# Kernel tuning notes

Hardware: AMD Instinct MI355X
Metric: run time of the kernel (lower is better)

Reference implementation:

```python
import jax, jax.numpy as jnp
import numpy as np

T, N, HIDDEN = 2048, 4, 512
N_HEAD = 8
D_HEAD = HIDDEN // N_HEAD
# Faithful to torch buffer: 1.0 / hidden_size ** d_head -> underflows to 0.0
SCALE = np.float32(1.0 / (HIDDEN ** D_HEAD))
LN_EPS = 1e-5


def _layernorm(x, g, b):
    m = jnp.mean(x, axis=-1, keepdims=True)
    v = jnp.mean(jnp.square(x - m), axis=-1, keepdims=True)
    return (x - m) * jax.lax.rsqrt(v + LN_EPS) * g + b


def setup_inputs() -> dict:
    key = jax.random.key(0)
    ks = jax.random.split(key, 6)
    s = 0.02
    return {
        "x": jax.random.normal(ks[0], (T, N, HIDDEN), jnp.float32),
        "qkv_w": jax.random.normal(ks[1], (HIDDEN, 3 * HIDDEN), jnp.float32) * s,
        "qkv_b": jnp.zeros((3 * HIDDEN,), jnp.float32),
        "out_w": jax.random.normal(ks[2], (HIDDEN, HIDDEN), jnp.float32) * s,
        "out_b": jnp.zeros((HIDDEN,), jnp.float32),
        "ln1_g": jnp.ones((HIDDEN,), jnp.float32),
        "ln1_b": jnp.zeros((HIDDEN,), jnp.float32),
        "ff1_w": jax.random.normal(ks[3], (HIDDEN, 2 * HIDDEN), jnp.float32) * s,
        "ff1_b": jnp.zeros((2 * HIDDEN,), jnp.float32),
        "ff2_w": jax.random.normal(ks[4], (2 * HIDDEN, HIDDEN), jnp.float32) * s,
        "ff2_b": jnp.zeros((HIDDEN,), jnp.float32),
        "ln2_g": jnp.ones((HIDDEN,), jnp.float32),
        "ln2_b": jnp.zeros((HIDDEN,), jnp.float32),
    }


def reference(x, qkv_w, qkv_b, out_w, out_b, ln1_g, ln1_b,
              ff1_w, ff1_b, ff2_w, ff2_b, ln2_g, ln2_b):
    t, n, _ = x.shape
    # prenorm=True path, dropout_p=0 (identity)
    residual = x
    h = _layernorm(x, ln1_g, ln1_b)
    qkv = h @ qkv_w + qkv_b  # [t, n, 3*hidden]
    q, k, v = jnp.split(qkv, 3, axis=2)
    q = q.reshape(t, n, N_HEAD, D_HEAD)
    k = k.reshape(t, n, N_HEAD, D_HEAD)
    v = v.reshape(t, n, N_HEAD, D_HEAD)
    logits = jnp.einsum('ibhd,jbhd->ijbh', q, k)
    probs = jax.nn.softmax(logits * SCALE, axis=1)
    attn_out = jnp.einsum('ijbh,jbhd->ibhd', probs, v).reshape(t, n, HIDDEN)
    x = residual + (attn_out @ out_w + out_b)
    residual = x
    h = _layernorm(x, ln2_g, ln2_b)
    ff = jnp.maximum(h @ ff1_w + ff1_b, 0.0) @ ff2_w + ff2_b
    return residual + ff
```

## Files before the change

### kernel.cpp

```cpp
#include <hip/hip_runtime.h>
#include <math.h>


#define DEVI __device__ __forceinline__

typedef unsigned short u16;
typedef unsigned int   u32;
using short8 = __attribute__((ext_vector_type(8))) short;
using f32x4  = __attribute__((ext_vector_type(4))) float;

constexpr int T_ = 2048;
constexpr int NB = 4;
constexpr int H  = 512;
constexpr int M  = T_ * NB;
constexpr int FF = 2 * H;
constexpr float LN_EPS = 1e-5f;

DEVI u16 f2bf(float f) {
    union { float f; u32 u; } v; v.f = f;
    u32 r = v.u + 0x7FFFu + ((v.u >> 16) & 1u);
    return (u16)(r >> 16);
}

DEVI void gload16(const u16* src, u16* lds) {
    __builtin_amdgcn_global_load_lds(
        (const __attribute__((address_space(1))) u32*)src,
        (__attribute__((address_space(3))) u32*)lds, 16, 0, 0);
}

DEVI float hsum8(const float4& a, const float4& b) {
    return a.x + a.y + a.z + a.w + b.x + b.y + b.z + b.w;
}
DEVI float hsq8(const float4& a, const float4& b) {
    return a.x*a.x + a.y*a.y + a.z*a.z + a.w*a.w +
           b.x*b.x + b.y*b.y + b.z*b.z + b.w*b.w;
}
DEVI float4 ln_apply(const float4& v, float mean, float rs,
                     const float4& g, const float4& b) {
    float4 r;
    r.x = (v.x - mean) * rs * g.x + b.x;
    r.y = (v.y - mean) * rs * g.y + b.y;
    r.z = (v.z - mean) * rs * g.z + b.z;
    r.w = (v.w - mean) * rs * g.w + b.w;
    return r;
}
DEVI void add4(float4& a, const float4& b) {
    a.x += b.x; a.y += b.y; a.z += b.z; a.w += b.w;
}
DEVI void wave_reduce2(float& s, float& q) {
    #pragma unroll
    for (int m = 1; m < 64; m <<= 1) {
        s += __shfl_xor(s, m, 64);
        q += __shfl_xor(q, m, 64);
    }
}

__global__ __launch_bounds__(256) void k_prep(
    const float* __restrict__ W1, const float* __restrict__ W2,
    u16* __restrict__ w1f, u16* __restrict__ w2f, float* __restrict__ mh)
{
    __shared__ float tile[32][33];
    const int t = threadIdx.x;
    const int bid = blockIdx.x;

    if (bid == 0) {
        for (int i = t; i < NB * H; i += 256) mh[i] = 0.f;
    }

    const float* W;
    u16* Wf;
    int K, N, k0, n0;
    if (bid < 512) {
        W = W1; Wf = w1f; K = H; N = FF;
        k0 = (bid & 15) * 32;  n0 = (bid >> 4) * 32;
    } else {
        const int b2 = bid - 512;
        W = W2; Wf = w2f; K = FF; N = H;
        k0 = (b2 & 31) * 32;   n0 = (b2 >> 5) * 32;
    }

    #pragma unroll
    for (int i = 0; i < 4; ++i) {
        const int idx = t + i * 256;
        const int r = idx >> 5, c = idx & 31;
        tile[r][c] = W[(size_t)(k0 + r) * N + n0 + c];
    }
    __syncthreads();
    if (t < 128) {
        const int tt = t >> 6;
        const int c  = t & 63;
        short8 o;
        #pragma unroll
        for (int kin = 0; kin < 8; ++kin)
            o[kin] = f2bf(tile[(c >> 4) * 8 + kin][tt * 16 + (c & 15)]);
        const size_t idx = (((size_t)(n0 / 16 + tt) * (K >> 5) + (k0 >> 5)) << 9)
                         + c * 8;
        *(short8*)&Wf[idx] = o;
    }
}

__global__ __launch_bounds__(256) void k_ln1_atomic(
    const float* __restrict__ x, const float* __restrict__ g,
    const float* __restrict__ be, float* __restrict__ mh)
{
    const int lane = threadIdx.x & 63;
    const int w    = threadIdx.x >> 6;
    const int t0   = blockIdx.x * 8;

    const float4* G4 = (const float4*)g;
    const float4* B4 = (const float4*)be;
    const float4 g0 = G4[lane], g1 = G4[64 + lane];
    const float4 b0 = B4[lane], b1 = B4[64 + lane];

    float4 acc0 = {0, 0, 0, 0}, acc1 = {0, 0, 0, 0};
    for (int i = 0; i < 8; ++i) {
        const int r = (t0 + i) * NB + w;
        const float4* X4 = (const float4*)(x + (size_t)r * H);
        float4 v0 = X4[lane], v1 = X4[64 + lane];
        float s = hsum8(v0, v1);
        float q = hsq8(v0, v1);
        wave_reduce2(s, q);
        const float mean = s * (1.0f / H);
        const float var  = q * (1.0f / H) - mean * mean;
        const float rs   = 1.0f / sqrtf(var + LN_EPS);
        add4(acc0, ln_apply(v0, mean, rs, g0, b0));
        add4(acc1, ln_apply(v1, mean, rs, g1, b1));
    }
    float* dst = mh + (size_t)w * H;
    atomicAdd(&dst[lane * 4 + 0],       acc0.x);
    atomicAdd(&dst[lane * 4 + 1],       acc0.y);
    atomicAdd(&dst[lane * 4 + 2],       acc0.z);
    atomicAdd(&dst[lane * 4 + 3],       acc0.w);
    atomicAdd(&dst[256 + lane * 4 + 0], acc1.x);
    atomicAdd(&dst[256 + lane * 4 + 1], acc1.y);
    atomicAdd(&dst[256 + lane * 4 + 2], acc1.z);
    atomicAdd(&dst[256 + lane * 4 + 3], acc1.w);
}

__global__ __launch_bounds__(256) void k_gemv_coal(
    const float* __restrict__ vec, const float* __restrict__ W,
    const float* __restrict__ bias, float* __restrict__ outv,
    const int Kd, const int stride, const int colofs, const float vscale)
{
    __shared__ float red[16][17];
    const int t  = threadIdx.x;
    const int b  = blockIdx.x >> 5;
    const int j0 = (blockIdx.x & 31) * 16;
    const int jj = t & 15, ks = t >> 4;

    const float* vp = vec + (size_t)b * Kd + ks * 32;
    const float* wp = W + (size_t)(ks * 32) * stride + colofs + j0 + jj;
    float acc = 0.f;
    #pragma unroll 8
    for (int i = 0; i < 32; ++i)
        acc = fmaf(vp[i] * vscale, wp[(size_t)i * stride], acc);

    red[ks][jj] = acc;
    __syncthreads();
    if (t < 16) {
        float s = 0.f;
        #pragma unroll
        for (int k2 = 0; k2 < 16; ++k2) s += red[k2][t];
        outv[(size_t)b * 512 + j0 + t] = s + bias[j0 + t];
    }
}

__global__ __launch_bounds__(256) void k_ln2(
    const float* __restrict__ x, const float* __restrict__ cvec,
    const float* __restrict__ g, const float* __restrict__ be,
    u16* __restrict__ h2f)
{
    const int lane = threadIdx.x & 63;
    const int w    = threadIdx.x >> 6;
    const int r    = blockIdx.x * 4 + w;
    const int b    = r & 3;

    const float4* X4 = (const float4*)(x + (size_t)r * H);
    const float4* C4 = (const float4*)(cvec + (size_t)b * H);
    float4 v0 = X4[lane * 2],     v1 = X4[lane * 2 + 1];
    add4(v0, C4[lane * 2]);
    add4(v1, C4[lane * 2 + 1]);

    float s = hsum8(v0, v1);
    float q = hsq8(v0, v1);
    wave_reduce2(s, q);
    const float mean = s * (1.0f / H);
    const float var  = q * (1.0f / H) - mean * mean;
    const float rs   = 1.0f / sqrtf(var + LN_EPS);

    const float4* G4 = (const float4*)g;
    const float4* B4 = (const float4*)be;
    float4 h0 = ln_apply(v0, mean, rs, G4[lane * 2],     B4[lane * 2]);
    float4 h1 = ln_apply(v1, mean, rs, G4[lane * 2 + 1], B4[lane * 2 + 1]);

    short8 o;
    o[0] = f2bf(h0.x); o[1] = f2bf(h0.y); o[2] = f2bf(h0.z); o[3] = f2bf(h0.w);
    o[4] = f2bf(h1.x); o[5] = f2bf(h1.y); o[6] = f2bf(h1.z); o[7] = f2bf(h1.w);

    const size_t idx = (((size_t)(r >> 4) * 16 + (lane >> 2)) << 9)
                     + ((lane & 3) * 16 + (r & 15)) * 8;
    *(short8*)&h2f[idx] = o;
}

template<int MODE>
__global__ __launch_bounds__(256) void gemm_bf16(
    const u16* __restrict__ Af, const u16* __restrict__ Bf,
    const float* __restrict__ bias,
    const float* __restrict__ resid_x, const float* __restrict__ resid_c,
    float* __restrict__ outf, u16* __restrict__ outfrag,
    const int K, const int N)
{
    constexpr int BM = 128, BN = 128, BK = 64;
    const int KT = K >> 5;
    __shared__ alignas(16) u16 As[BM * BK];
    __shared__ alignas(16) u16 Bs[BN * BK];

    const int t    = threadIdx.x;
    const int lane = t & 63, w = t >> 6;
    const int wr = w >> 1, wc = w & 1;
    const int lr = lane & 15, lk = lane >> 4;
    const int bmt = blockIdx.x * 8;
    const int bnt = blockIdx.y * 8;

    f32x4 acc[4][4];
    #pragma unroll
    for (int i = 0; i < 4; ++i)
        #pragma unroll
        for (int j = 0; j < 4; ++j)
            acc[i][j] = (f32x4){0.f, 0.f, 0.f, 0.f};

    for (int kt0 = 0; kt0 < KT; kt0 += 2) {
        __syncthreads();
        #pragma unroll
        for (int ft = 0; ft < 4; ++ft) {
            const int f = ft * 256 + t;
            const int mt = f >> 7, ktl = (f >> 6) & 1, c = f & 63;
            gload16(Af + (((size_t)(bmt + mt) * KT + kt0 + ktl) << 9) + c * 8,
                    &As[f * 8]);
        }
        #pragma unroll
        for (int ft = 0; ft < 4; ++ft) {
            const int f = ft * 256 + t;
            const int nt = f >> 7, ktl = (f >> 6) & 1, c = f & 63;
            gload16(Bf + (((size_t)(bnt + nt) * KT + kt0 + ktl) << 9) + c * 8,
                    &Bs[f * 8]);
        }
        __syncthreads();

        #pragma unroll
        for (int ktl = 0; ktl < 2; ++ktl) {
            short8 a[4], b[4];
            #pragma unroll
            for (int i = 0; i < 4; ++i)
                a[i] = *(const short8*)&As[(((wr * 4 + i) * 2 + ktl) << 9) + lane * 8];
            #pragma unroll
            for (int j = 0; j < 4; ++j)
                b[j] = *(const short8*)&Bs[(((wc * 4 + j) * 2 + ktl) << 9) + lane * 8];
            #pragma unroll
            for (int i = 0; i < 4; ++i)
                #pragma unroll
                for (int j = 0; j < 4; ++j)
                    acc[i][j] = __builtin_amdgcn_mfma_f32_16x16x32_bf16(
                        a[i], b[j], acc[i][j], 0, 0, 0);
        }
    }

    const int K2T = N >> 5;
    #pragma unroll
    for (int i = 0; i < 4; ++i) {
        const int rt   = bmt + wr * 4 + i;
        const int row0 = rt * 16 + lk * 4;
        #pragma unroll
        for (int j = 0; j < 4; ++j) {
            const int col = (bnt + wc * 4 + j) * 16 + lr;
            const float bv = bias[col];
            #pragma unroll
            for (int r = 0; r < 4; ++r) {
                const int row = row0 + r;
                float v = acc[i][j][r] + bv;
                if (MODE == 0) {
                    v = fmaxf(v, 0.f);
                    const size_t idx =
                        (((size_t)rt * K2T + (col >> 5)) << 9)
                        + (((col >> 3) & 3) * 16 + (lk * 4 + r)) * 8
                        + (col & 7);
                    outfrag[idx] = f2bf(v);
                } else {
                    v += resid_x[(size_t)row * N + col]
                       + resid_c[(row & 3) * N + col];
                    outf[(size_t)row * N + col] = v;
                }
            }
        }
    }
}

extern "C" void kernel_launch(void* const* d_in, const int* in_sizes, int n_in,
                              void* d_out, int out_size, void* d_ws, size_t ws_size,
                              hipStream_t stream)
{
    const float* x     = (const float*)d_in[0];
    const float* qkv_w = (const float*)d_in[1];
    const float* qkv_b = (const float*)d_in[2];
    const float* out_w = (const float*)d_in[3];
    const float* out_b = (const float*)d_in[4];
    const float* ln1_g = (const float*)d_in[5];
    const float* ln1_b = (const float*)d_in[6];
    const float* ff1_w = (const float*)d_in[7];
    const float* ff1_b = (const float*)d_in[8];
    const float* ff2_w = (const float*)d_in[9];
    const float* ff2_b = (const float*)d_in[10];
    const float* ln2_g = (const float*)d_in[11];
    const float* ln2_b = (const float*)d_in[12];

    float* out = (float*)d_out;

    float* fws   = (float*)d_ws;
    float* mh    = fws;
    float* vmean = mh + NB * H;
    float* cvec  = vmean + NB * H;
    u16*   h2f   = (u16*)(cvec + NB * H);
    u16*   f1f   = h2f + (size_t)M * H;
    u16*   w1f   = f1f + (size_t)M * FF;
    u16*   w2f   = w1f + (size_t)H * FF;

    k_prep<<<1024, 256, 0, stream>>>(ff1_w, ff2_w, w1f, w2f, mh);

    k_ln1_atomic<<<256, 256, 0, stream>>>(x, ln1_g, ln1_b, mh);

    k_gemv_coal<<<128, 256, 0, stream>>>(mh, qkv_w, qkv_b + 2 * H, vmean,
                                         H, 3 * H, 2 * H, 1.0f / T_);
    k_gemv_coal<<<128, 256, 0, stream>>>(vmean, out_w, out_b, cvec,
                                         H, H, 0, 1.0f);

    k_ln2<<<M / 4, 256, 0, stream>>>(x, cvec, ln2_g, ln2_b, h2f);

    gemm_bf16<0><<<dim3(M / 128, FF / 128), 256, 0, stream>>>(
        h2f, w1f, ff1_b, nullptr, nullptr, nullptr, f1f, H, FF);

    gemm_bf16<1><<<dim3(M / 128, H / 128), 256, 0, stream>>>(
        f1f, w2f, ff2_b, x, cvec, out, nullptr, FF, H);
}
```

Measured before the change: 176.9 us.

## Merge prep kernels into one launch and precompute fused V·out weight

Combines the weight conversion, LN1 column-sum reduction, and a new precomputation of Wv@Wout (plus the fused bias) into a single multi-role kernel. Atomics are replaced by per-chunk partial sums that a new gemv kernel reduces. That kernel then applies the fused 512x512 weight in one pass instead of two chained gemvs. This cuts four launches down to two and removes the serial gemv dependency. The cost is an extra 512^3 FLOP fp32 matmul on every call and a 256-chunk partial reduction per batch column.

```diff
diff --git a/kernel.cpp b/kernel.cpp
--- a/kernel.cpp
+++ b/kernel.cpp
@@ -15,6 +15,7 @@
 constexpr int M  = T_ * NB;
 constexpr int FF = 2 * H;
 constexpr float LN_EPS = 1e-5f;
+constexpr int NCHUNK = 256;
 
 DEVI u16 f2bf(float f) {
     union { float f; u32 u; } v; v.f = f;
@@ -55,105 +56,156 @@
     }
 }
 
-__global__ __launch_bounds__(256) void k_prep(
+constexpr int NW1  = 512;
+constexpr int NW2  = 512;
+constexpr int NWE  = 256;
+constexpr int NBE  = 2;
+constexpr int NLN  = 256;
+constexpr int MEGA_BLOCKS = NW1 + NW2 + NWE + NBE + NLN;
+
+__global__ __launch_bounds__(256) void k_mega(
     const float* __restrict__ W1, const float* __restrict__ W2,
-    u16* __restrict__ w1f, u16* __restrict__ w2f, float* __restrict__ mh)
-{
-    __shared__ float tile[32][33];
-    const int t = threadIdx.x;
+    const float* __restrict__ qkv_w, const float* __restrict__ qkv_b,
+    const float* __restrict__ out_w, const float* __restrict__ out_b,
+    const float* __restrict__ x, const float* __restrict__ ln1g,
+    const float* __restrict__ ln1b,
+    u16* __restrict__ w1f, u16* __restrict__ w2f,
+    float* __restrict__ Weff, float* __restrict__ beff,
+    float* __restrict__ partials)
+{
+    __shared__ float smem[2 * 32 * 33];
+    const int t   = threadIdx.x;
     const int bid = blockIdx.x;
 
-    if (bid == 0) {
-        for (int i = t; i < NB * H; i += 256) mh[i] = 0.f;
-    }
-
-    const float* W;
-    u16* Wf;
-    int K, N, k0, n0;
-    if (bid < 512) {
-        W = W1; Wf = w1f; K = H; N = FF;
-        k0 = (bid & 15) * 32;  n0 = (bid >> 4) * 32;
+    if (bid < NW1 + NW2) {
+        const float* W;
+        u16* Wf;
+        int K, N, k0, n0;
+        if (bid < NW1) {
+            W = W1; Wf = w1f; K = H; N = FF;
+            k0 = (bid & 15) * 32;  n0 = (bid >> 4) * 32;
+        } else {
+            const int b2 = bid - NW1;
+            W = W2; Wf = w2f; K = FF; N = H;
+            k0 = (b2 & 31) * 32;   n0 = (b2 >> 5) * 32;
+        }
+        #pragma unroll
+        for (int i = 0; i < 4; ++i) {
+            const int idx = t + i * 256;
+            const int r = idx >> 5, c = idx & 31;
+            smem[r * 33 + c] = W[(size_t)(k0 + r) * N + n0 + c];
+        }
+        __syncthreads();
+        if (t < 128) {
+            const int tt = t >> 6;
+            const int c  = t & 63;
+            short8 o;
+            #pragma unroll
+            for (int kin = 0; kin < 8; ++kin)
+                o[kin] = f2bf(smem[((c >> 4) * 8 + kin) * 33 + tt * 16 + (c & 15)]);
+            const size_t idx =
+                (((size_t)(n0 / 16 + tt) * (K >> 5) + (k0 >> 5)) << 9) + c * 8;
+            *(short8*)&Wf[idx] = o;
+        }
+    } else if (bid < NW1 + NW2 + NWE) {
+        const int b3 = bid - (NW1 + NW2);
+        const int kt = b3 & 15, jt = b3 >> 4;
+        float* Av = smem;
+        float* Bo = smem + 32 * 33;
+        const int r  = t >> 3;
+        const int c4 = (t & 7) * 4;
+        float acc[4] = {0.f, 0.f, 0.f, 0.f};
+        for (int qt = 0; qt < 16; ++qt) {
+            #pragma unroll
+            for (int i = 0; i < 4; ++i) {
+                const int idx = t + i * 256;
+                const int rr = idx >> 5, cc = idx & 31;
+                Av[rr * 33 + cc] =
+                    qkv_w[(size_t)(kt * 32 + rr) * 1536 + 1024 + qt * 32 + cc];
+                Bo[rr * 33 + cc] =
+                    out_w[(size_t)(qt * 32 + rr) * 512 + jt * 32 + cc];
+            }
+            __syncthreads();
+            #pragma unroll 8
+            for (int q = 0; q < 32; ++q) {
+                const float a = Av[r * 33 + q];
+                acc[0] = fmaf(a, Bo[q * 33 + c4 + 0], acc[0]);
+                acc[1] = fmaf(a, Bo[q * 33 + c4 + 1], acc[1]);
+                acc[2] = fmaf(a, Bo[q * 33 + c4 + 2], acc[2]);
+                acc[3] = fmaf(a, Bo[q * 33 + c4 + 3], acc[3]);
+            }
+            __syncthreads();
+        }
+        #pragma unroll
+        for (int i = 0; i < 4; ++i)
+            Weff[(size_t)(kt * 32 + r) * 512 + jt * 32 + c4 + i] = acc[i];
+    } else if (bid < NW1 + NW2 + NWE + NBE) {
+        const int j = (bid - (NW1 + NW2 + NWE)) * 256 + t;
+        smem[t]       = qkv_b[1024 + t];
+        smem[256 + t] = qkv_b[1280 + t];
+        __syncthreads();
+        float acc = out_b[j];
+        #pragma unroll 8
+        for (int k = 0; k < 512; ++k)
+            acc = fmaf(smem[k], out_w[(size_t)k * 512 + j], acc);
+        beff[j] = acc;
     } else {
-        const int b2 = bid - 512;
-        W = W2; Wf = w2f; K = FF; N = H;
-        k0 = (b2 & 31) * 32;   n0 = (b2 >> 5) * 32;
-    }
-
-    #pragma unroll
-    for (int i = 0; i < 4; ++i) {
-        const int idx = t + i * 256;
-        const int r = idx >> 5, c = idx & 31;
-        tile[r][c] = W[(size_t)(k0 + r) * N + n0 + c];
-    }
-    __syncthreads();
-    if (t < 128) {
-        const int tt = t >> 6;
-        const int c  = t & 63;
-        short8 o;
-        #pragma unroll
-        for (int kin = 0; kin < 8; ++kin)
-            o[kin] = f2bf(tile[(c >> 4) * 8 + kin][tt * 16 + (c & 15)]);
-        const size_t idx = (((size_t)(n0 / 16 + tt) * (K >> 5) + (k0 >> 5)) << 9)
-                         + c * 8;
-        *(short8*)&Wf[idx] = o;
-    }
-}
-
-__global__ __launch_bounds__(256) void k_ln1_atomic(
-    const float* __restrict__ x, const float* __restrict__ g,
-    const float* __restrict__ be, float* __restrict__ mh)
-{
-    const int lane = threadIdx.x & 63;
-    const int w    = threadIdx.x >> 6;
-    const int t0   = blockIdx.x * 8;
-
-    const float4* G4 = (const float4*)g;
-    const float4* B4 = (const float4*)be;
-    const float4 g0 = G4[lane], g1 = G4[64 + lane];
-    const float4 b0 = B4[lane], b1 = B4[64 + lane];
-
-    float4 acc0 = {0, 0, 0, 0}, acc1 = {0, 0, 0, 0};
-    for (int i = 0; i < 8; ++i) {
-        const int r = (t0 + i) * NB + w;
-        const float4* X4 = (const float4*)(x + (size_t)r * H);
-        float4 v0 = X4[lane], v1 = X4[64 + lane];
-        float s = hsum8(v0, v1);
-        float q = hsq8(v0, v1);
-        wave_reduce2(s, q);
-        const float mean = s * (1.0f / H);
-        const float var  = q * (1.0f / H) - mean * mean;
-        const float rs   = 1.0f / sqrtf(var + LN_EPS);
-        add4(acc0, ln_apply(v0, mean, rs, g0, b0));
-        add4(acc1, ln_apply(v1, mean, rs, g1, b1));
-    }
-    float* dst = mh + (size_t)w * H;
-    atomicAdd(&dst[lane * 4 + 0],       acc0.x);
-    atomicAdd(&dst[lane * 4 + 1],       acc0.y);
-    atomicAdd(&dst[lane * 4 + 2],       acc0.z);
-    atomicAdd(&dst[lane * 4 + 3],       acc0.w);
-    atomicAdd(&dst[256 + lane * 4 + 0], acc1.x);
-    atomicAdd(&dst[256 + lane * 4 + 1], acc1.y);
-    atomicAdd(&dst[256 + lane * 4 + 2], acc1.z);
-    atomicAdd(&dst[256 + lane * 4 + 3], acc1.w);
-}
-
-__global__ __launch_bounds__(256) void k_gemv_coal(
-    const float* __restrict__ vec, const float* __restrict__ W,
-    const float* __restrict__ bias, float* __restrict__ outv,
-    const int Kd, const int stride, const int colofs, const float vscale)
-{
+        const int lb   = bid - (NW1 + NW2 + NWE + NBE);
+        const int lane = t & 63;
+        const int w    = t >> 6;
+        const int t0   = lb * 8;
+
+        const float4* G4 = (const float4*)ln1g;
+        const float4* B4 = (const float4*)ln1b;
+        const float4 g0 = G4[lane], g1 = G4[64 + lane];
+        const float4 b0 = B4[lane], b1 = B4[64 + lane];
+
+        float4 acc0 = {0, 0, 0, 0}, acc1 = {0, 0, 0, 0};
+        for (int i = 0; i < 8; ++i) {
+            const int r = (t0 + i) * NB + w;
+            const float4* X4 = (const float4*)(x + (size_t)r * H);
+            float4 v0 = X4[lane], v1 = X4[64 + lane];
+            float s = hsum8(v0, v1);
+            float q = hsq8(v0, v1);
+            wave_reduce2(s, q);
+            const float mean = s * (1.0f / H);
+            const float var  = q * (1.0f / H) - mean * mean;
+            const float rs   = 1.0f / sqrtf(var + LN_EPS);
+            add4(acc0, ln_apply(v0, mean, rs, g0, b0));
+            add4(acc1, ln_apply(v1, mean, rs, g1, b1));
+        }
+        float4* P4 = (float4*)(partials + ((size_t)w * NCHUNK + lb) * H);
+        P4[lane]      = acc0;
+        P4[64 + lane] = acc1;
+    }
+}
+
+__global__ __launch_bounds__(256) void k_gemv_eff(
+    const float* __restrict__ partials, const float* __restrict__ Weff,
+    const float* __restrict__ beff, float* __restrict__ cvec)
+{
+    __shared__ float mh[512];
     __shared__ float red[16][17];
     const int t  = threadIdx.x;
     const int b  = blockIdx.x >> 5;
     const int j0 = (blockIdx.x & 31) * 16;
+
+    float s0 = 0.f, s1 = 0.f;
+    const float* P = partials + (size_t)b * NCHUNK * H;
+    for (int c = 0; c < NCHUNK; ++c) {
+        s0 += P[(size_t)c * H + t];
+        s1 += P[(size_t)c * H + 256 + t];
+    }
+    mh[t]       = s0 * (1.0f / T_);
+    mh[256 + t] = s1 * (1.0f / T_);
+    __syncthreads();
+
     const int jj = t & 15, ks = t >> 4;
-
-    const float* vp = vec + (size_t)b * Kd + ks * 32;
-    const float* wp = W + (size_t)(ks * 32) * stride + colofs + j0 + jj;
+    const float* wp = Weff + (size_t)(ks * 32) * 512 + j0 + jj;
     float acc = 0.f;
     #pragma unroll 8
     for (int i = 0; i < 32; ++i)
-        acc = fmaf(vp[i] * vscale, wp[(size_t)i * stride], acc);
+        acc = fmaf(mh[ks * 32 + i], wp[(size_t)i * 512], acc);
 
     red[ks][jj] = acc;
     __syncthreads();
@@ -161,7 +213,7 @@
         float s = 0.f;
         #pragma unroll
         for (int k2 = 0; k2 < 16; ++k2) s += red[k2][t];
-        outv[(size_t)b * 512 + j0 + t] = s + bias[j0 + t];
+        cvec[(size_t)b * 512 + j0 + t] = s + beff[j0 + t];
     }
 }
 
@@ -315,23 +367,21 @@
 
     float* out = (float*)d_out;
 
-    float* fws   = (float*)d_ws;
-    float* mh    = fws;
-    float* vmean = mh + NB * H;
-    float* cvec  = vmean + NB * H;
-    u16*   h2f   = (u16*)(cvec + NB * H);
-    u16*   f1f   = h2f + (size_t)M * H;
-    u16*   w1f   = f1f + (size_t)M * FF;
-    u16*   w2f   = w1f + (size_t)H * FF;
-
-    k_prep<<<1024, 256, 0, stream>>>(ff1_w, ff2_w, w1f, w2f, mh);
-
-    k_ln1_atomic<<<256, 256, 0, stream>>>(x, ln1_g, ln1_b, mh);
-
-    k_gemv_coal<<<128, 256, 0, stream>>>(mh, qkv_w, qkv_b + 2 * H, vmean,
-                                         H, 3 * H, 2 * H, 1.0f / T_);
-    k_gemv_coal<<<128, 256, 0, stream>>>(vmean, out_w, out_b, cvec,
-                                         H, H, 0, 1.0f);
+    float* fws      = (float*)d_ws;
+    float* partials = fws;
+    float* Weff     = partials + (size_t)NB * NCHUNK * H;
+    float* beff     = Weff + (size_t)H * H;
+    float* cvec     = beff + H;
+    u16*   h2f      = (u16*)(cvec + NB * H);
+    u16*   f1f      = h2f + (size_t)M * H;
+    u16*   w1f      = f1f + (size_t)M * FF;
+    u16*   w2f      = w1f + (size_t)H * FF;
+
+    k_mega<<<MEGA_BLOCKS, 256, 0, stream>>>(
+        ff1_w, ff2_w, qkv_w, qkv_b, out_w, out_b, x, ln1_g, ln1_b,
+        w1f, w2f, Weff, beff, partials);
+
+    k_gemv_eff<<<128, 256, 0, stream>>>(partials, Weff, beff, cvec);
 
     k_ln2<<<M / 4, 256, 0, stream>>>(x, cvec, ln2_g, ln2_b, h2f);
 
```

New measurement: 170.3 us. 1.04x faster.
